# Kernel optimization log

Hardware: AMD Instinct MI355X
Metric: run time of the kernel (lower is better)

The kernel has to match this reference:

```python
import jax, jax.numpy as jnp
import numpy as np

H = 512   # GRU hidden size
D = 300   # word embedding size
Z = 128   # conditioning dim


def _gru_cell(x, h, Wih, Whh, bih, bhh):
    # torch.nn.GRUCell semantics
    gi = x @ Wih.T + bih          # [B, 3H]
    gh = h @ Whh.T + bhh          # [B, 3H]
    ir, iz, inn = jnp.split(gi, 3, axis=-1)
    hr, hz, hn = jnp.split(gh, 3, axis=-1)
    r = jax.nn.sigmoid(ir + hr)
    z = jax.nn.sigmoid(iz + hz)
    n = jnp.tanh(inn + r * hn)
    return (1.0 - z) * n + z * h


def setup_inputs() -> dict:
    key = jax.random.key(0)
    ks = jax.random.split(key, 16)
    B, S = 1024, 64
    text = jax.random.normal(ks[0], (B, S, D), jnp.float32)
    text_lengths = jax.random.randint(ks[1], (B,), 1, S + 1)  # >=1 avoids div-by-zero
    s = 1.0 / np.sqrt(H)

    def u(k, shape):
        return jax.random.uniform(k, shape, jnp.float32, -s, s)

    return {
        "text": text,
        "text_lengths": text_lengths,
        "Wih_f": u(ks[2], (3 * H, D)), "Whh_f": u(ks[3], (3 * H, H)),
        "bih_f": u(ks[4], (3 * H,)),   "bhh_f": u(ks[5], (3 * H,)),
        "Wih_b": u(ks[6], (3 * H, D)), "Whh_b": u(ks[7], (3 * H, H)),
        "bih_b": u(ks[8], (3 * H,)),   "bhh_b": u(ks[9], (3 * H,)),
        "W_mu": u(ks[10], (Z, H)),  "b_mu": u(ks[11], (Z,)),
        "W_sig": u(ks[12], (Z, H)), "b_sig": u(ks[13], (Z,)),
        "eps": jax.random.normal(ks[14], (B, Z), jnp.float32),
    }


def reference(text, text_lengths, Wih_f, Whh_f, bih_f, bhh_f,
              Wih_b, Whh_b, bih_b, bhh_b, W_mu, b_mu, W_sig, b_sig, eps):
    B, S, _ = text.shape
    xs = jnp.transpose(text, (1, 0, 2))                       # [S, B, D]
    mask = (jnp.arange(S)[:, None] < text_lengths[None, :]).astype(text.dtype)  # [S, B]
    h0 = jnp.zeros((B, H), text.dtype)

    def fstep(h, inp):
        x, m = inp
        h = _gru_cell(x, h, Wih_f, Whh_f, bih_f, bhh_f)
        return h, h * m[:, None]

    _, hf = jax.lax.scan(fstep, h0, (xs, mask))               # [S, B, H]

    def bstep(h, inp):
        x, m = inp
        h = _gru_cell(x, h, Wih_b, Whh_b, bih_b, bhh_b)
        return h, h * m[:, None]

    # backward pass reads text[-i-1] and masks with the FORWARD-index mask (as in original)
    _, hb_seq = jax.lax.scan(bstep, h0, (xs[::-1], mask))     # [S, B, H]
    # original stores backward step i at index (-i) mod S:
    # out[j] = hb_seq[(S - j) % S]  ==  roll(reverse(hb_seq), 1)
    hb = jnp.roll(hb_seq[::-1], 1, axis=0)

    words = (hf + hb) * 0.5                                   # [S, B, H]
    avg = words.sum(0) / mask.sum(0)[:, None]                 # [B, H]

    lrelu = lambda v: jnp.where(v >= 0, v, 0.2 * v)
    mu = lrelu(avg @ W_mu.T + b_mu)                           # [B, Z]
    sigma = jnp.exp(lrelu(avg @ W_sig.T + b_sig))             # [B, Z]
    final = eps * sigma + mu                                  # reparameterized sample
    return (final, mu, sigma)
```

## Files before the change

kernel.cpp:

```cpp
#include <hip/hip_runtime.h>

#define B_ 1024
#define S_ 64
#define D_ 300
#define DP_ 320
#define H_ 512
#define G3_ 1536
#define Z_ 128
#define NC1 10
#define NC2 16
#define CSTR 64

typedef __bf16 bf16x8 __attribute__((ext_vector_type(8)));
typedef float f32x4 __attribute__((ext_vector_type(4)));

#define GLLD(g, l) __builtin_amdgcn_global_load_lds( \
    (const __attribute__((address_space(1))) void*)(g), \
    (__attribute__((address_space(3))) void*)(l), 16, 0, 0)
#define GLLD_SYS(g, l) __builtin_amdgcn_global_load_lds( \
    (const __attribute__((address_space(1))) void*)(g), \
    (__attribute__((address_space(3))) void*)(l), 16, 0, 17)

#define MFMA(a, b, c) __builtin_amdgcn_mfma_f32_16x16x32_bf16((a), (b), (c), 0, 0, 0)

__global__ __launch_bounds__(256) void prep_cnt(unsigned* __restrict__ cnt) {
    int i = blockIdx.x * 256 + threadIdx.x;
    cnt[i] = 0u;
}

__global__ __launch_bounds__(320) void prep_text(const float* __restrict__ text,
                                                 __bf16* __restrict__ Xbf) {
    int bs = blockIdx.x;
    int b = bs >> 6, s = bs & 63;
    int dp = threadIdx.x;
    float v = (dp < D_) ? text[(size_t)bs * D_ + dp] : 0.f;
    Xbf[((size_t)s * B_ + b) * DP_ + dp] = (__bf16)v;
}

__global__ __launch_bounds__(256) void prep_w(
    const float* __restrict__ Wih_f, const float* __restrict__ Whh_f,
    const float* __restrict__ Wih_b, const float* __restrict__ Whh_b,
    const float* __restrict__ W_mu, const float* __restrict__ W_sig,
    __bf16* __restrict__ Wk1, __bf16* __restrict__ Wk2, __bf16* __restrict__ Wcat) {
    const int n1 = 2 * G3_ * DP_;
    const int n2 = 2 * G3_ * H_;
    int i = blockIdx.x * 256 + threadIdx.x;
    if (i < n1) {
        int dir = i / (G3_ * DP_);
        int rem = i - dir * (G3_ * DP_);
        int r = rem / DP_;
        int k = rem - r * DP_;
        const float* W = dir ? Wih_b : Wih_f;
        Wk1[i] = (k < D_) ? (__bf16)W[(size_t)r * D_ + k] : (__bf16)0.f;
    } else if (i < n1 + n2) {
        int jj = i - n1;
        int dir = jj / (G3_ * H_);
        int rem = jj - dir * (G3_ * H_);
        int r = rem / H_;
        int k = rem - r * H_;
        const float* W = dir ? Whh_b : Whh_f;
        Wk2[jj] = (__bf16)W[(size_t)r * H_ + k];
    } else {
        int idx = i - n1 - n2;
        int z = idx >> 9, k = idx & 511;
        Wcat[idx] = (__bf16)(z < 128 ? W_mu[(size_t)z * H_ + k]
                                     : W_sig[(size_t)(z - 128) * H_ + k]);
    }
}

__global__ __launch_bounds__(256, 1) void gru_persist(
    const __bf16* __restrict__ Xbf, const __bf16* __restrict__ Wk1,
    const __bf16* __restrict__ Wk2,
    const float* __restrict__ bih_f, const float* __restrict__ bhh_f,
    const float* __restrict__ bih_b, const float* __restrict__ bhh_b,
    const int* __restrict__ lens,
    __bf16* __restrict__ Hb0, __bf16* __restrict__ Hb1,
    float* __restrict__ Ssum, unsigned* __restrict__ cnt)
{
    __shared__ __align__(16) __bf16 hbuf[NC2 * 2048];
    __shared__ __align__(16) __bf16 xbuf[2 * NC1 * 2048];

    const int bid = blockIdx.x;
    const int xcd = bid & 7, slot = bid >> 3;
    const int dir = xcd >> 2;
    const int mb  = (xcd & 3) * 4 + (slot >> 3);
    const int jb  = slot & 7;
    const int b0  = mb * 64;
    const int group = dir * 16 + mb;
    unsigned* const gcnt = cnt + group * CSTR;

    const int tid = threadIdx.x;
    const int wave = tid >> 6;
    const int lane = tid & 63;

    const int jcol = jb * 64 + wave * 16 + (lane & 15);
    const int kq8  = (lane >> 4) * 8;

    const int srow = tid >> 2;
    const int scol = ((tid & 3) ^ ((tid >> 3) & 3)) * 8;
    const size_t hrow = (size_t)(dir * B_ + b0 + srow) * H_ + scol;

    {
        const int sx0 = dir ? (S_ - 1) : 0;
        const __bf16* src = Xbf + ((size_t)sx0 * B_ + b0 + srow) * DP_ + scol;
        __bf16* dst = xbuf + wave * 512;
#pragma unroll
        for (int c = 0; c < NC1; ++c)
            GLLD(src + c * 32, dst + c * 2048);
    }

    bf16x8 w1c[NC1][3];
    bf16x8 w2c[NC2][3];
    {
        const __bf16* w1p[3];
        const __bf16* w2p[3];
#pragma unroll
        for (int g = 0; g < 3; ++g) {
            w1p[g] = Wk1 + ((size_t)dir * G3_ + g * H_ + jcol) * DP_ + kq8;
            w2p[g] = Wk2 + ((size_t)dir * G3_ + g * H_ + jcol) * H_ + kq8;
        }
#pragma unroll
        for (int c = 0; c < NC1; ++c)
#pragma unroll
            for (int g = 0; g < 3; ++g)
                w1c[c][g] = *(const bf16x8*)(w1p[g] + c * 32);
#pragma unroll
        for (int c = 0; c < NC2; ++c)
#pragma unroll
            for (int g = 0; g < 3; ++g)
                w2c[c][g] = *(const bf16x8*)(w2p[g] + c * 32);
    }

    const float* bih = dir ? bih_b : bih_f;
    const float* bhh = dir ? bhh_b : bhh_f;
    const float b_r  = bih[jcol] + bhh[jcol];
    const float b_z  = bih[H_ + jcol] + bhh[H_ + jcol];
    const float b_ni = bih[2 * H_ + jcol];
    const float b_nh = bhh[2 * H_ + jcol];

    unsigned lenp[4];
#pragma unroll
    for (int mt = 0; mt < 4; ++mt) {
        int r0 = b0 + mt * 16 + (lane >> 4) * 4;
        lenp[mt] = (unsigned)(lens[r0] & 255) | ((unsigned)(lens[r0 + 1] & 255) << 8)
                 | ((unsigned)(lens[r0 + 2] & 255) << 16) | ((unsigned)(lens[r0 + 3] & 255) << 24);
    }

    float hreg[16], ssum[16];
#pragma unroll
    for (int i = 0; i < 16; ++i) { hreg[i] = 0.f; ssum[i] = 0.f; }

    const int qsl  = (lane >> 4) ^ ((lane >> 1) & 3);
    const int aoff = (lane & 15) * 32 + qsl * 8;

#define LDX(P, c) do { _Pragma("unroll") \
    for (int mt_ = 0; mt_ < 4; ++mt_) \
        P[mt_] = *(const bf16x8*)(xb + (c) * 2048 + aoff + mt_ * 512); } while (0)
#define LDH(P, c) do { _Pragma("unroll") \
    for (int mt_ = 0; mt_ < 4; ++mt_) \
        P[mt_] = *(const bf16x8*)(hbuf + (c) * 2048 + aoff + mt_ * 512); } while (0)
#define FMA1(P, c) do { _Pragma("unroll") \
    for (int mt_ = 0; mt_ < 4; ++mt_) { \
        acc[mt_][0] = MFMA(P[mt_], w1c[c][0], acc[mt_][0]); \
        acc[mt_][1] = MFMA(P[mt_], w1c[c][1], acc[mt_][1]); \
        acc[mt_][2] = MFMA(P[mt_], w1c[c][2], acc[mt_][2]); } } while (0)
#define FMA2(P, c) do { _Pragma("unroll") \
    for (int mt_ = 0; mt_ < 4; ++mt_) { \
        acc[mt_][0] = MFMA(P[mt_], w2c[c][0], acc[mt_][0]); \
        acc[mt_][1] = MFMA(P[mt_], w2c[c][1], acc[mt_][1]); \
        acc[mt_][3] = MFMA(P[mt_], w2c[c][2], acc[mt_][3]); } } while (0)
#define XDMA(snext) do { \
    const int sxn_ = dir ? (S_ - 1 - (snext)) : (snext); \
    const __bf16* src_ = Xbf + ((size_t)sxn_ * B_ + b0 + srow) * DP_ + scol; \
    __bf16* dst_ = xbuf + ((snext) & 1) * (NC1 * 2048) + wave * 512; \
    _Pragma("unroll") \
    for (int c_ = 0; c_ < NC1; ++c_) \
        GLLD(src_ + c_ * 32, dst_ + c_ * 2048); } while (0)

    __syncthreads();

    for (int s = 0; s < S_; ++s) {
        if (s == 0) XDMA(1);

        f32x4 acc[4][4];
#pragma unroll
        for (int mt = 0; mt < 4; ++mt)
#pragma unroll
            for (int p = 0; p < 4; ++p)
                acc[mt][p] = (f32x4){0.f, 0.f, 0.f, 0.f};

        const __bf16* xb = xbuf + (s & 1) * (NC1 * 2048);
        bf16x8 pa[4], pb[4];

        LDX(pa, 0); LDX(pb, 1);
        FMA1(pa, 0); LDX(pa, 2);
        FMA1(pb, 1); LDX(pb, 3);
        FMA1(pa, 2); LDX(pa, 4);
        FMA1(pb, 3); LDX(pb, 5);

        if (s > 0) {
            if (tid == 0) {
                const unsigned tgt = 8u * (unsigned)s;
                unsigned it = 0;
                while (__hip_atomic_load(gcnt, __ATOMIC_RELAXED,
                                         __HIP_MEMORY_SCOPE_AGENT) < tgt) {
                    if (++it > (1u << 20)) break;
                }
            }
            __syncthreads();

            {
                const __bf16* src = ((s & 1) ? Hb1 : Hb0) + hrow;
                __bf16* dst = hbuf + wave * 512;
#pragma unroll
                for (int c = 0; c < NC2; ++c)
                    GLLD_SYS(src + c * 32, dst + c * 2048);
            }
        }

        FMA1(pa, 4); LDX(pa, 6);
        FMA1(pb, 5); LDX(pb, 7);
        FMA1(pa, 6); LDX(pa, 8);
        FMA1(pb, 7); LDX(pb, 9);
        FMA1(pa, 8);
        FMA1(pb, 9);

        if (s > 0) {
            __syncthreads();

            if (s < S_ - 1) XDMA(s + 1);

            LDH(pa, 0); LDH(pb, 1);
#pragma unroll
            for (int cc = 0; cc < 7; ++cc) {
                FMA2(pa, 2 * cc);     LDH(pa, 2 * cc + 2);
                FMA2(pb, 2 * cc + 1); LDH(pb, 2 * cc + 3);
            }
            FMA2(pa, 14);
            FMA2(pb, 15);
        }

        {
            __bf16* hb_w = (s & 1) ? Hb0 : Hb1;
            const bool store_lane = (lane & 1) == 0;
#pragma unroll
            for (int mt = 0; mt < 4; ++mt) {
#pragma unroll
                for (int reg = 0; reg < 4; ++reg) {
                    const int i = mt * 4 + reg;
                    const float r = 1.f / (1.f + __expf(-(acc[mt][0][reg] + b_r)));
                    const float z = 1.f / (1.f + __expf(-(acc[mt][1][reg] + b_z)));
                    const float nv = acc[mt][2][reg] + b_ni + r * (acc[mt][3][reg] + b_nh);
                    const float n = 2.f / (1.f + __expf(-2.f * nv)) - 1.f;
                    const float hnew = (1.f - z) * n + z * hreg[i];
                    hreg[i] = hnew;
                    if (((lenp[mt] >> (reg * 8)) & 255u) > (unsigned)s) ssum[i] += hnew;
                    __bf16 hb16 = (__bf16)hnew;
                    unsigned short myb = __builtin_bit_cast(unsigned short, hb16);
                    unsigned ob = (unsigned)__shfl_xor((int)(unsigned)myb, 1, 64);
                    if (store_lane) {
                        const int b = b0 + mt * 16 + (lane >> 4) * 4 + reg;
                        __hip_atomic_store(
                            (unsigned*)(hb_w + (size_t)(dir * B_ + b) * H_ + jcol),
                            (unsigned)myb | (ob << 16),
                            __ATOMIC_RELAXED, __HIP_MEMORY_SCOPE_AGENT);
                    }
                }
            }
        }
        __syncthreads();
        if (tid == 0 && s < S_ - 1)
            __hip_atomic_fetch_add(gcnt, 1u, __ATOMIC_RELAXED,
                                   __HIP_MEMORY_SCOPE_AGENT);
    }

#undef LDX
#undef LDH
#undef FMA1
#undef FMA2
#undef XDMA

#pragma unroll
    for (int mt = 0; mt < 4; ++mt)
#pragma unroll
        for (int reg = 0; reg < 4; ++reg) {
            const int b = b0 + mt * 16 + (lane >> 4) * 4 + reg;
            Ssum[(size_t)(dir * B_ + b) * H_ + jcol] = ssum[mt * 4 + reg];
        }
}

__global__ __launch_bounds__(128) void avg_prep(const float* __restrict__ Ssum,
                                                const int* __restrict__ lens,
                                                __bf16* __restrict__ Avg) {
    int b = blockIdx.x, t = threadIdx.x;
    float inv = 0.5f / (float)lens[b];
    float4 a = *(const float4*)(Ssum + (size_t)b * H_ + t * 4);
    float4 c = *(const float4*)(Ssum + (size_t)(B_ + b) * H_ + t * 4);
    __bf16* dst = Avg + (size_t)b * H_ + t * 4;
    dst[0] = (__bf16)((a.x + c.x) * inv);
    dst[1] = (__bf16)((a.y + c.y) * inv);
    dst[2] = (__bf16)((a.z + c.z) * inv);
    dst[3] = (__bf16)((a.w + c.w) * inv);
}

__global__ __launch_bounds__(256) void head_gemm(
    const __bf16* __restrict__ Avg, const __bf16* __restrict__ Wcat,
    const float* __restrict__ b_mu, const float* __restrict__ b_sig,
    float* __restrict__ out)
{
    __shared__ __align__(16) __bf16 abuf[16 * 2048];
    const int bid = blockIdx.x;
    const int mb = bid >> 2, jb = bid & 3;
    const int tid = threadIdx.x, wave = tid >> 6, lane = tid & 63;
    const int srow = tid >> 2, scol = (tid & 3) * 8;
    const __bf16* asrc = Avg + (size_t)(mb * 64 + srow) * H_ + scol;
    {
        __bf16* dst = abuf + wave * 512;
#pragma unroll
        for (int c = 0; c < 16; ++c) GLLD(asrc + c * 32, dst + c * 2048);
    }
    __syncthreads();
    const int j = jb * 64 + wave * 16 + (lane & 15);
    const int kq8 = (lane >> 4) * 8;
    const __bf16* wp = Wcat + (size_t)j * H_ + kq8;
    const int aoff = (lane & 15) * 32 + kq8;
    f32x4 acc[4];
#pragma unroll
    for (int mt = 0; mt < 4; ++mt) acc[mt] = (f32x4){0.f, 0.f, 0.f, 0.f};
#pragma unroll
    for (int c = 0; c < 16; ++c) {
        bf16x8 wf = *(const bf16x8*)(wp + c * 32);
#pragma unroll
        for (int mt = 0; mt < 4; ++mt) {
            bf16x8 af = *(const bf16x8*)(abuf + c * 2048 + aoff + mt * 512);
            acc[mt] = MFMA(af, wf, acc[mt]);
        }
    }
    const int gate = j >> 7, z = j & 127;
    const float bias = gate ? b_sig[z] : b_mu[z];
#pragma unroll
    for (int mt = 0; mt < 4; ++mt)
#pragma unroll
        for (int reg = 0; reg < 4; ++reg) {
            const int b = mb * 64 + mt * 16 + (lane >> 4) * 4 + reg;
            float v = acc[mt][reg] + bias;
            v = v >= 0.f ? v : 0.2f * v;
            if (gate) v = __expf(v);
            out[(size_t)(1 + gate) * B_ * Z_ + (size_t)b * Z_ + z] = v;
        }
}

__global__ __launch_bounds__(256) void final_k(const float* __restrict__ eps,
                                               float* __restrict__ out) {
    int i = blockIdx.x * 256 + threadIdx.x;
    out[i] = eps[i] * out[2 * B_ * Z_ + i] + out[B_ * Z_ + i];
}

extern "C" void kernel_launch(void* const* d_in, const int* in_sizes, int n_in,
                              void* d_out, int out_size, void* d_ws, size_t ws_size,
                              hipStream_t stream) {
    const float* text  = (const float*)d_in[0];
    const int*   lens  = (const int*)  d_in[1];
    const float* Wih_f = (const float*)d_in[2];
    const float* Whh_f = (const float*)d_in[3];
    const float* bih_f = (const float*)d_in[4];
    const float* bhh_f = (const float*)d_in[5];
    const float* Wih_b = (const float*)d_in[6];
    const float* Whh_b = (const float*)d_in[7];
    const float* bih_b = (const float*)d_in[8];
    const float* bhh_b = (const float*)d_in[9];
    const float* W_mu  = (const float*)d_in[10];
    const float* b_mu  = (const float*)d_in[11];
    const float* W_sig = (const float*)d_in[12];
    const float* b_sig = (const float*)d_in[13];
    const float* eps   = (const float*)d_in[14];
    float* out = (float*)d_out;

    char* ws = (char*)d_ws;
    __bf16* Xbf  = (__bf16*)(ws);
    __bf16* Wk1  = (__bf16*)(ws + 41943040);
    __bf16* Wk2  = (__bf16*)(ws + 43909120);
    __bf16* Hb0  = (__bf16*)(ws + 47054848);
    __bf16* Hb1  = (__bf16*)(ws + 49152000);
    float*  Ssum = (float*) (ws + 51249152);
    __bf16* Avg  = (__bf16*)(ws + 55443456);
    __bf16* Wcat = (__bf16*)(ws + 56492032);
    unsigned* cntp = (unsigned*)(ws + 56754176);

    prep_cnt<<<8, 256, 0, stream>>>(cntp);
    prep_text<<<B_ * S_, 320, 0, stream>>>(text, Xbf);
    prep_w<<<10496, 256, 0, stream>>>(Wih_f, Whh_f, Wih_b, Whh_b, W_mu, W_sig,
                                      Wk1, Wk2, Wcat);

    void* args[] = { (void*)&Xbf, (void*)&Wk1, (void*)&Wk2,
                     (void*)&bih_f, (void*)&bhh_f, (void*)&bih_b, (void*)&bhh_b,
                     (void*)&lens, (void*)&Hb0, (void*)&Hb1,
                     (void*)&Ssum, (void*)&cntp };
    hipError_t ce = hipLaunchCooperativeKernel((void*)gru_persist, dim3(256),
                                               dim3(256), args, 0, stream);
    if (ce != hipSuccess) {
        gru_persist<<<256, 256, 0, stream>>>(Xbf, Wk1, Wk2,
                                             bih_f, bhh_f, bih_b, bhh_b,
                                             lens, Hb0, Hb1, Ssum, cntp);
    }

    avg_prep<<<B_, 128, 0, stream>>>(Ssum, lens, Avg);
    head_gemm<<<64, 256, 0, stream>>>(Avg, Wcat, b_mu, b_sig, out);
    final_k<<<512, 256, 0, stream>>>(eps, out);
}
```

Before: 839.6 us.

## Triple-buffer fragment loads and split hidden-state DMA wait into two halves

Operand fragments now rotate through three register buffers instead of two, so more LDS reads are in flight ahead of each MFMA group. The full __syncthreads before the recurrent GEMM is replaced by explicit vmcnt waits plus raw barriers. The first half of the hidden-state chunks can be consumed while the second half of the global-to-LDS DMA is still arriving. This relies on hand-counted vmcnt values matching the number of outstanding loads, which is fragile and could race if the compiler reorders or the count is wrong.

```diff
diff --git a/kernel.cpp b/kernel.cpp
--- a/kernel.cpp
+++ b/kernel.cpp
@@ -22,6 +22,9 @@
     (__attribute__((address_space(3))) void*)(l), 16, 0, 17)
 
 #define MFMA(a, b, c) __builtin_amdgcn_mfma_f32_16x16x32_bf16((a), (b), (c), 0, 0, 0)
+
+#define SBAR() __builtin_amdgcn_s_barrier()
+#define SFENCE() __builtin_amdgcn_sched_barrier(0)
 
 __global__ __launch_bounds__(256) void prep_cnt(unsigned* __restrict__ cnt) {
     int i = blockIdx.x * 256 + threadIdx.x;
@@ -190,13 +193,11 @@
                 acc[mt][p] = (f32x4){0.f, 0.f, 0.f, 0.f};
 
         const __bf16* xb = xbuf + (s & 1) * (NC1 * 2048);
-        bf16x8 pa[4], pb[4];
-
-        LDX(pa, 0); LDX(pb, 1);
-        FMA1(pa, 0); LDX(pa, 2);
-        FMA1(pb, 1); LDX(pb, 3);
-        FMA1(pa, 2); LDX(pa, 4);
-        FMA1(pb, 3); LDX(pb, 5);
+        bf16x8 pa[4], pb[4], pc[4];
+
+        LDX(pa, 0); LDX(pb, 1); LDX(pc, 2);
+        FMA1(pa, 0); LDX(pa, 3);
+        FMA1(pb, 1); LDX(pb, 4);
 
         if (s > 0) {
             if (tid == 0) {
@@ -218,24 +219,47 @@
             }
         }
 
-        FMA1(pa, 4); LDX(pa, 6);
-        FMA1(pb, 5); LDX(pb, 7);
-        FMA1(pa, 6); LDX(pa, 8);
-        FMA1(pb, 7); LDX(pb, 9);
-        FMA1(pa, 8);
-        FMA1(pb, 9);
+        FMA1(pc, 2); LDX(pc, 5);
+        FMA1(pa, 3); LDX(pa, 6);
+        FMA1(pb, 4); LDX(pb, 7);
+        FMA1(pc, 5); LDX(pc, 8);
+        FMA1(pa, 6); LDX(pa, 9);
+        FMA1(pb, 7);
+        FMA1(pc, 8);
+        FMA1(pa, 9);
 
         if (s > 0) {
-            __syncthreads();
-
-            if (s < S_ - 1) XDMA(s + 1);
-
-            LDH(pa, 0); LDH(pb, 1);
-#pragma unroll
-            for (int cc = 0; cc < 7; ++cc) {
-                FMA2(pa, 2 * cc);     LDH(pa, 2 * cc + 2);
-                FMA2(pb, 2 * cc + 1); LDH(pb, 2 * cc + 3);
+            if (s < S_ - 1) {
+                XDMA(s + 1);
+                asm volatile("s_waitcnt vmcnt(18)" ::: "memory");
+            } else {
+                asm volatile("s_waitcnt vmcnt(8)" ::: "memory");
             }
+            SBAR(); SFENCE();
+
+            LDH(pa, 0); LDH(pb, 1); LDH(pc, 2);
+            FMA2(pa, 0); LDH(pa, 3);
+            FMA2(pb, 1); LDH(pb, 4);
+            FMA2(pc, 2); LDH(pc, 5);
+            FMA2(pa, 3); LDH(pa, 6);
+            FMA2(pb, 4); LDH(pb, 7);
+            FMA2(pc, 5);
+            FMA2(pa, 6);
+            FMA2(pb, 7);
+
+            if (s < S_ - 1)
+                asm volatile("s_waitcnt vmcnt(10)" ::: "memory");
+            else
+                asm volatile("s_waitcnt vmcnt(0)" ::: "memory");
+            SBAR(); SFENCE();
+
+            LDH(pa, 8); LDH(pb, 9); LDH(pc, 10);
+            FMA2(pa, 8);  LDH(pa, 11);
+            FMA2(pb, 9);  LDH(pb, 12);
+            FMA2(pc, 10); LDH(pc, 13);
+            FMA2(pa, 11); LDH(pa, 14);
+            FMA2(pb, 12); LDH(pb, 15);
+            FMA2(pc, 13);
             FMA2(pa, 14);
             FMA2(pb, 15);
         }
```

New measurement: 843.6 us. About the same (+0.5%).
